# Performance work log

Measured on AMD Instinct MI355X. Metric: run time of the kernel, lower is better.

## Reference

```python
import jax, jax.numpy as jnp
import numpy as np

IN_FEATURES = 512
NUM_TREES = 512
DEPTH = 5
NLEAF = 2 ** DEPTH
RESPONSE_DIM = 1
BATCH = 2048


def make_path_map():
    # OBLIVIOUS_map from DeTree.InitPathWay: nodes[j] = j (oblivious tree),
    # index 2*node + bit into the flattened [depth, 2] choice tensor.
    path = []
    for no in range(NLEAF):
        b = no
        for j in range(DEPTH):
            path.append(2 * j + (b % 2))
            b //= 2
    return np.asarray(path, dtype=np.int32)  # [NLEAF * DEPTH]


def setup_inputs() -> dict:
    key = jax.random.key(0)
    k1, k2, k3, k4, k5 = jax.random.split(key, 5)
    x = jax.random.normal(k1, (BATCH, IN_FEATURES), dtype=jnp.float32)
    # nn.init.uniform_ on [in_features, num_trees * depth]
    feat_attention = jax.random.uniform(k2, (IN_FEATURES, NUM_TREES * DEPTH), dtype=jnp.float32)
    feature_thresholds = jax.random.normal(k3, (NUM_TREES, DEPTH), dtype=jnp.float32)
    log_temperatures = jax.random.normal(k4, (NUM_TREES, DEPTH), dtype=jnp.float32) * 0.1
    response = jax.random.normal(k5, (NUM_TREES, RESPONSE_DIM, NLEAF), dtype=jnp.float32)
    path_map = jnp.asarray(make_path_map())
    return {"x": x, "feat_attention": feat_attention,
            "feature_thresholds": feature_thresholds,
            "log_temperatures": log_temperatures,
            "response": response, "path_map": path_map}


def reference(x, feat_attention, feature_thresholds, log_temperatures, response, path_map):
    B, F = x.shape
    n, d = feature_thresholds.shape
    # feature gating: softmax over the feature axis (dim=0)
    choice_weight = jax.nn.softmax(feat_attention, axis=0).reshape(F, n, d)
    feature_values = jnp.einsum('bf,fnd->bnd', x, choice_weight)  # [B, n, d]
    # temperature-scaled split logits
    tl = (feature_values - feature_thresholds) * jnp.exp(-log_temperatures)
    logits = jnp.stack([-tl, tl], axis=-1)  # [B, n, d, 2]
    # sparsemoid binary gate
    choice = jnp.clip(0.5 * logits + 0.5, 0.0, 1.0)
    # route through tree paths: gather per-leaf path gates, product along depth
    gate = choice.reshape(B, n, d * 2)[:, :, path_map].reshape(B, n, -1, d)
    bins_prob = jnp.prod(gate, axis=-1)  # [B, n, nLeaf]
    out = jnp.einsum('bnl,ncl->bnc', bins_prob, response)  # [B, n, response_dim]
    return out.reshape(B, -1)  # flatten_output=True
```

## Files before the change

kernel.cpp:

```cpp
#include <hip/hip_runtime.h>
#include <hip/hip_bf16.h>

#define F_DIM 512
#define NT 512
#define DEPTH 5
#define NCOL (NT * DEPTH)
#define BATCH 2048

typedef __attribute__((ext_vector_type(8))) short bf16x8;
typedef __attribute__((ext_vector_type(4))) float f32x4;

__device__ __forceinline__ void gl2lds16(const void* g, void* l) {
    __builtin_amdgcn_global_load_lds((const __attribute__((address_space(1))) void*)g,
                                     (__attribute__((address_space(3))) void*)l,
                                     16, 0, 0);
}

__global__ __launch_bounds__(256) void prep(const float* __restrict__ x,
                                            const float* __restrict__ fa,
                                            __hip_bfloat16* __restrict__ Xb,
                                            __hip_bfloat16* __restrict__ Wt) {
    if (blockIdx.x < 1024) {
        const size_t i = (size_t)blockIdx.x * 256 + threadIdx.x;
        const float4 v = ((const float4*)x)[i];
        union { ushort4 u; __hip_bfloat16 h[4]; } pk;
        pk.h[0] = __float2bfloat16(v.x);
        pk.h[1] = __float2bfloat16(v.y);
        pk.h[2] = __float2bfloat16(v.z);
        pk.h[3] = __float2bfloat16(v.w);
        ((ushort4*)Xb)[i] = pk.u;
        return;
    }
    const int bx = blockIdx.x - 1024;
    const int l = threadIdx.x & 15;
    const int g = threadIdx.x >> 4;
    const int col = bx * 16 + l;
    const int f0 = g * 32;
    __shared__ float red[16][16];

    float e[32];
    float s = 0.f;
#pragma unroll
    for (int i = 0; i < 32; ++i) {
        e[i] = __expf(fa[(size_t)(f0 + i) * NCOL + col]);
        s += e[i];
    }
    red[g][l] = s;
    __syncthreads();

    float S = 0.f;
#pragma unroll
    for (int gg = 0; gg < 16; ++gg) S += red[gg][l];
    const float inv = 1.0f / S;

    __hip_bfloat16* dst = Wt + (size_t)col * F_DIM + f0;
#pragma unroll
    for (int i = 0; i < 32; i += 4) {
        union { ushort4 u; __hip_bfloat16 h[4]; } pk;
#pragma unroll
        for (int jj = 0; jj < 4; ++jj)
            pk.h[jj] = __float2bfloat16(e[i + jj] * inv);
        *(ushort4*)(dst + i) = pk.u;
    }
}

__global__ __launch_bounds__(256, 2) void gemm_tree(const __hip_bfloat16* __restrict__ A,
                                                    const __hip_bfloat16* __restrict__ Bt,
                                                    const float* __restrict__ th,
                                                    const float* __restrict__ lt,
                                                    const float* __restrict__ resp,
                                                    float* __restrict__ out) {
    __shared__ __align__(16) char smem[28672];
    __hip_bfloat16* As = (__hip_bfloat16*)smem;
    __hip_bfloat16* Bs = (__hip_bfloat16*)(smem + 8192);
    float* E = (float*)smem;

    const int tid = threadIdx.x;
    const int w = tid >> 6;
    const int l = tid & 63;
    const int m0 = blockIdx.y * 64;
    const int n0c = blockIdx.x * 160;
    const int n0t = blockIdx.x * 32;
    const int wm = (w & 1) * 32;
    const int wn = (w >> 1) * 80;

    f32x4 acc[2][5] = {};

    const int srow = l >> 3;
    const int schunk = (l & 7) ^ srow;

    for (int kt = 0; kt < 8; ++kt) {
        const int k0 = kt * 64;
#pragma unroll
        for (int q = 0; q < 2; ++q) {
            const int g = q * 4 + w;
            gl2lds16(A + ((size_t)(m0 + g * 8 + srow) * F_DIM + k0 + schunk * 8),
                     As + g * 8 * 64);
        }
#pragma unroll
        for (int q = 0; q < 5; ++q) {
            const int g = q * 4 + w;
            gl2lds16(Bt + ((size_t)(n0c + g * 8 + srow) * F_DIM + k0 + schunk * 8),
                     Bs + g * 8 * 64);
        }
        __syncthreads();

#pragma unroll
        for (int ks = 0; ks < 2; ++ks) {
            const int cb = ks * 4 + (l >> 4);
            bf16x8 af[2], bfr[5];
#pragma unroll
            for (int im = 0; im < 2; ++im) {
                const int r = wm + im * 16 + (l & 15);
                af[im] = *(const bf16x8*)(As + r * 64 + ((cb ^ (r & 7)) * 8));
            }
#pragma unroll
            for (int in = 0; in < 5; ++in) {
                const int r = wn + in * 16 + (l & 15);
                bfr[in] = *(const bf16x8*)(Bs + r * 64 + ((cb ^ (r & 7)) * 8));
            }
#pragma unroll
            for (int im = 0; im < 2; ++im)
#pragma unroll
                for (int in = 0; in < 5; ++in)
                    acc[im][in] = __builtin_amdgcn_mfma_f32_16x16x32_bf16(
                        af[im], bfr[in], acc[im][in], 0, 0, 0);
        }
        __syncthreads();
    }

    const int tree = tid & 31;
    const int rg = tid >> 5;
    const int gt = n0t + tree;

    float al[DEPTH], be[DEPTH];
#pragma unroll
    for (int j = 0; j < DEPTH; ++j) {
        const float a = 0.5f * __expf(-lt[gt * DEPTH + j]);
        al[j] = a;
        be[j] = 0.5f - th[gt * DEPTH + j] * a;
    }
    float rs[32];
#pragma unroll
    for (int i = 0; i < 32; ++i) rs[i] = resp[gt * 32 + i];

    const int PAD = 161;
#pragma unroll
    for (int im = 0; im < 2; ++im) {
#pragma unroll
        for (int in = 0; in < 5; ++in) {
            const int scol = wn + in * 16 + (l & 15);
#pragma unroll
            for (int r = 0; r < 4; ++r) {
                const int sr = (w & 1) * 16 + (l >> 4) * 4 + r;
                E[sr * PAD + scol] = acc[im][in][r];
            }
        }
        __syncthreads();

#pragma unroll
        for (int rr = 0; rr < 4; ++rr) {
            const int s = rg * 4 + rr;
            const int gb = m0 + ((s < 16) ? (im * 16 + s) : (32 + im * 16 + (s - 16)));
            const float* f = E + s * PAD + tree * 5;
            float c1[DEPTH];
#pragma unroll
            for (int j = 0; j < DEPTH; ++j) {
                const float v = fmaf(al[j], f[j], be[j]);
                c1[j] = fminf(fmaxf(v, 0.f), 1.f);
            }
            float s16[16], s8[8], s4[4], s2[2];
#pragma unroll
            for (int m = 0; m < 16; ++m) s16[m] = fmaf(c1[0], rs[2*m+1] - rs[2*m], rs[2*m]);
#pragma unroll
            for (int m = 0; m < 8; ++m)  s8[m]  = fmaf(c1[1], s16[2*m+1] - s16[2*m], s16[2*m]);
#pragma unroll
            for (int m = 0; m < 4; ++m)  s4[m]  = fmaf(c1[2], s8[2*m+1] - s8[2*m], s8[2*m]);
#pragma unroll
            for (int m = 0; m < 2; ++m)  s2[m]  = fmaf(c1[3], s4[2*m+1] - s4[2*m], s4[2*m]);
            out[(size_t)gb * NT + gt] = fmaf(c1[4], s2[1] - s2[0], s2[0]);
        }
        __syncthreads();
    }
}

extern "C" void kernel_launch(void* const* d_in, const int* in_sizes, int n_in,
                              void* d_out, int out_size, void* d_ws, size_t ws_size,
                              hipStream_t stream) {
    const float* x    = (const float*)d_in[0];
    const float* fa   = (const float*)d_in[1];
    const float* th   = (const float*)d_in[2];
    const float* lt   = (const float*)d_in[3];
    const float* resp = (const float*)d_in[4];

    char* ws = (char*)d_ws;
    __hip_bfloat16* Wt = (__hip_bfloat16*)(ws);
    __hip_bfloat16* Xb = (__hip_bfloat16*)(ws + (4u << 20));
    float* out = (float*)d_out;

    hipLaunchKernelGGL(prep, dim3(1024 + 160), dim3(256), 0, stream, x, fa, Xb, Wt);
    hipLaunchKernelGGL(gemm_tree, dim3(NCOL / 160, BATCH / 64), dim3(256), 0, stream,
                       Xb, Wt, th, lt, resp, out);
}
```

Before: 83.64 us.

## Double-buffer GEMM LDS tiles and widen softmax prep blocks

The GEMM main loop now double-buffers its A/B LDS tiles. It issues the next k-tile's global-to-LDS loads before computing on the current one, using explicit vmcnt waits and raw s_barriers instead of two __syncthreads per iteration. The prep kernel moves to 512-thread blocks that handle 32 softmax columns each, and it writes bf16 output in 16-byte stores. LDS per block doubles to 56 KB, which may limit occupancy to two blocks per CU, and correctness now depends on the hand-counted vmcnt value.

New measurement: 82.14 us, median of 2. About the same (-1.8%).

```diff
diff --git a/kernel.cpp b/kernel.cpp
--- a/kernel.cpp
+++ b/kernel.cpp
@@ -16,12 +16,12 @@
                                      16, 0, 0);
 }
 
-__global__ __launch_bounds__(256) void prep(const float* __restrict__ x,
+__global__ __launch_bounds__(512) void prep(const float* __restrict__ x,
                                             const float* __restrict__ fa,
                                             __hip_bfloat16* __restrict__ Xb,
                                             __hip_bfloat16* __restrict__ Wt) {
-    if (blockIdx.x < 1024) {
-        const size_t i = (size_t)blockIdx.x * 256 + threadIdx.x;
+    if (blockIdx.x >= 80) {
+        const size_t i = (size_t)(blockIdx.x - 80) * 512 + threadIdx.x;
         const float4 v = ((const float4*)x)[i];
         union { ushort4 u; __hip_bfloat16 h[4]; } pk;
         pk.h[0] = __float2bfloat16(v.x);
@@ -31,12 +31,11 @@
         ((ushort4*)Xb)[i] = pk.u;
         return;
     }
-    const int bx = blockIdx.x - 1024;
-    const int l = threadIdx.x & 15;
-    const int g = threadIdx.x >> 4;
-    const int col = bx * 16 + l;
+    const int l = threadIdx.x & 31;
+    const int g = threadIdx.x >> 5;
+    const int col = blockIdx.x * 32 + l;
     const int f0 = g * 32;
-    __shared__ float red[16][16];
+    __shared__ float red[16][32];
 
     float e[32];
     float s = 0.f;
@@ -55,12 +54,12 @@
 
     __hip_bfloat16* dst = Wt + (size_t)col * F_DIM + f0;
 #pragma unroll
-    for (int i = 0; i < 32; i += 4) {
-        union { ushort4 u; __hip_bfloat16 h[4]; } pk;
-#pragma unroll
-        for (int jj = 0; jj < 4; ++jj)
+    for (int i = 0; i < 32; i += 8) {
+        union { uint4 u; __hip_bfloat16 h[8]; } pk;
+#pragma unroll
+        for (int jj = 0; jj < 8; ++jj)
             pk.h[jj] = __float2bfloat16(e[i + jj] * inv);
-        *(ushort4*)(dst + i) = pk.u;
+        *(uint4*)(dst + i) = pk.u;
     }
 }
 
@@ -70,10 +69,7 @@
                                                     const float* __restrict__ lt,
                                                     const float* __restrict__ resp,
                                                     float* __restrict__ out) {
-    __shared__ __align__(16) char smem[28672];
-    __hip_bfloat16* As = (__hip_bfloat16*)smem;
-    __hip_bfloat16* Bs = (__hip_bfloat16*)(smem + 8192);
-    float* E = (float*)smem;
+    __shared__ __align__(16) char smem[57344];
 
     const int tid = threadIdx.x;
     const int w = tid >> 6;
@@ -89,22 +85,39 @@
     const int srow = l >> 3;
     const int schunk = (l & 7) ^ srow;
 
-    for (int kt = 0; kt < 8; ++kt) {
+    auto stage = [&](int kt, int buf) {
         const int k0 = kt * 64;
+        char* base = smem + buf * 28672;
 #pragma unroll
         for (int q = 0; q < 2; ++q) {
             const int g = q * 4 + w;
             gl2lds16(A + ((size_t)(m0 + g * 8 + srow) * F_DIM + k0 + schunk * 8),
-                     As + g * 8 * 64);
+                     base + g * 8 * 64 * 2);
         }
 #pragma unroll
         for (int q = 0; q < 5; ++q) {
             const int g = q * 4 + w;
             gl2lds16(Bt + ((size_t)(n0c + g * 8 + srow) * F_DIM + k0 + schunk * 8),
-                     Bs + g * 8 * 64);
-        }
-        __syncthreads();
-
+                     base + 8192 + g * 8 * 64 * 2);
+        }
+    };
+
+    stage(0, 0);
+#pragma unroll
+    for (int kt = 0; kt < 8; ++kt) {
+        const int cur = kt & 1;
+        __builtin_amdgcn_sched_barrier(0);
+        if (kt < 7) {
+            stage(kt + 1, cur ^ 1);
+            asm volatile("s_waitcnt vmcnt(7)" ::: "memory");
+        } else {
+            asm volatile("s_waitcnt vmcnt(0)" ::: "memory");
+        }
+        __builtin_amdgcn_s_barrier();
+        __builtin_amdgcn_sched_barrier(0);
+
+        const __hip_bfloat16* As = (const __hip_bfloat16*)(smem + cur * 28672);
+        const __hip_bfloat16* Bs = As + 4096;
 #pragma unroll
         for (int ks = 0; ks < 2; ++ks) {
             const int cb = ks * 4 + (l >> 4);
@@ -126,9 +139,12 @@
                     acc[im][in] = __builtin_amdgcn_mfma_f32_16x16x32_bf16(
                         af[im], bfr[in], acc[im][in], 0, 0, 0);
         }
-        __syncthreads();
-    }
-
+        __builtin_amdgcn_sched_barrier(0);
+        __builtin_amdgcn_s_barrier();
+    }
+    __builtin_amdgcn_sched_barrier(0);
+
+    float* E = (float*)smem;
     const int tree = tid & 31;
     const int rg = tid >> 5;
     const int gt = n0t + tree;
@@ -198,7 +214,7 @@
     __hip_bfloat16* Xb = (__hip_bfloat16*)(ws + (4u << 20));
     float* out = (float*)d_out;
 
-    hipLaunchKernelGGL(prep, dim3(1024 + 160), dim3(256), 0, stream, x, fa, Xb, Wt);
+    hipLaunchKernelGGL(prep, dim3(80 + 512), dim3(512), 0, stream, x, fa, Xb, Wt);
     hipLaunchKernelGGL(gemm_tree, dim3(NCOL / 160, BATCH / 64), dim3(256), 0, stream,
                        Xb, Wt, th, lt, resp, out);
 }
```
